# Kernel optimization log

Hardware: AMD Instinct MI355X
Metric: run time of the kernel (lower is better)

## Reference

```python
import jax, jax.numpy as jnp
import numpy as np

N_EMBD = 1024
HEAD_SIZE = 64


def setup_inputs() -> dict:
    key = jax.random.key(0)
    k1, k2, k3, k4 = jax.random.split(key, 4)
    x = jax.random.normal(k1, (8, 2048, N_EMBD), dtype=jnp.float32)
    # torch Linear(n_embd, head_size, bias=False): y = x @ W.T with W [out,in].
    # Store as [in, out] so y = x @ W. Scale init like torch default (~1/sqrt(in)).
    s = 1.0 / np.sqrt(N_EMBD)
    Wk = jax.random.uniform(k2, (N_EMBD, HEAD_SIZE), jnp.float32, -s, s)
    Wq = jax.random.uniform(k3, (N_EMBD, HEAD_SIZE), jnp.float32, -s, s)
    Wv = jax.random.uniform(k4, (N_EMBD, HEAD_SIZE), jnp.float32, -s, s)
    return {"x": x, "Wk": Wk, "Wq": Wq, "Wv": Wv}


def reference(x, Wk, Wq, Wv):
    # x: [B,T,C]
    B, T, C = x.shape
    k = x @ Wk  # [B,T,H]
    q = x @ Wq  # [B,T,H]
    v = x @ Wv  # [B,T,H]
    scale = HEAD_SIZE ** -0.5
    wei = jnp.einsum('bth,bsh->bts', q, k) * scale  # [B,T,T]
    causal = jnp.tril(jnp.ones((T, T), dtype=bool))  # [T,T]
    wei = jnp.where(causal[None, :, :], wei, -jnp.inf)
    wei = jax.nn.softmax(wei, axis=-1)
    # dropout(p=0.2) is identity in eval mode (deterministic baseline)
    out = jnp.einsum('bts,bsh->bth', wei, v)  # [B,T,H]
    return out
```

## Files before the change

kernel.cpp:

```cpp
#include <hip/hip_runtime.h>
#include <hip/hip_bf16.h>

#define B_DIM 8
#define T_DIM 2048
#define C_DIM 1024
#define H_DIM 64
#define BT (B_DIM * T_DIM)

typedef __attribute__((ext_vector_type(8))) short bf16x8;
typedef __attribute__((ext_vector_type(4))) float f32x4;

__device__ __forceinline__ ushort f2bf(float f) {
    __hip_bfloat16 h = __float2bfloat16(f);
    return *reinterpret_cast<ushort*>(&h);
}
__device__ __forceinline__ unsigned int packbf(float a, float b) {
    return (unsigned int)f2bf(a) | ((unsigned int)f2bf(b) << 16);
}

__global__ __launch_bounds__(256) void wt_convert_kernel(
    const float* __restrict__ Wk, const float* __restrict__ Wq,
    const float* __restrict__ Wv, ushort* __restrict__ wt)
{
    __shared__ float tile[64][65];
    const int mat = blockIdx.x >> 4;
    const int s   = blockIdx.x & 15;
    const int k0  = s << 6;
    const float* src = (mat == 0) ? Wk : (mat == 1) ? Wq : Wv;
    const float scale = (mat == 1) ? 0.125f * 1.4426950408889634f : 1.0f;
    #pragma unroll
    for (int i = 0; i < 16; ++i) {
        const int idx = i * 256 + threadIdx.x;
        const int r = idx >> 6, c = idx & 63;
        tile[r][c] = src[(size_t)(k0 + r) * H_DIM + c];
    }
    __syncthreads();
    const int ntl = threadIdx.x >> 6, lane = threadIdx.x & 63;
    const int col = lane & 15, quad = lane >> 4;
    const int nt = mat * 4 + ntl;
    const int w = nt / 3, j = nt % 3;
    #pragma unroll
    for (int ks = 0; ks < 2; ++ks) {
        unsigned int u[4];
        #pragma unroll
        for (int p = 0; p < 4; ++p)
            u[p] = packbf(tile[ks * 32 + quad * 8 + 2 * p][ntl * 16 + col] * scale,
                          tile[ks * 32 + quad * 8 + 2 * p + 1][ntl * 16 + col] * scale);
        ushort* dst = wt + (size_t)((((s * 4 + w) * 3 + j) * 2 + ks) * 512) + lane * 8;
        *(uint4*)dst = (uint4){u[0], u[1], u[2], u[3]};
    }
}

__global__ __launch_bounds__(256) void qkv_gemm_kernel(
    const float* __restrict__ x, const ushort* __restrict__ wt,
    ushort* __restrict__ kb, ushort* __restrict__ qb, ushort* __restrict__ vt)
{
    __shared__ ushort Xf[2][4 * 64 * 8];
    const int tid = threadIdx.x;
    const int wave = tid >> 6, lane = tid & 63;
    const int col = lane & 15, quad = lane >> 4;
    const int r0 = blockIdx.x * 32;

    f32x4 acc[2][3];
    #pragma unroll
    for (int m = 0; m < 2; ++m)
        #pragma unroll
        for (int i = 0; i < 3; ++i) acc[m][i] = (f32x4){0.f, 0.f, 0.f, 0.f};

    const int xrow = (wave >> 1) * 16 + col;
    const int xcc  = (wave & 1) * 4 + quad;
    const float* xsrc = x + (size_t)(r0 + xrow) * C_DIM + xcc * 8;

    const ushort* wsrc[3][2];
    #pragma unroll
    for (int j = 0; j < 3; ++j)
        #pragma unroll
        for (int ks = 0; ks < 2; ++ks)
            wsrc[j][ks] = wt + (size_t)(((wave * 3 + j) * 2 + ks) * 512) + lane * 8;

    {
        const float4 f0 = *(const float4*)(xsrc);
        const float4 f1 = *(const float4*)(xsrc + 4);
        uint4 u;
        u.x = packbf(f0.x, f0.y); u.y = packbf(f0.z, f0.w);
        u.z = packbf(f1.x, f1.y); u.w = packbf(f1.z, f1.w);
        *(uint4*)&Xf[0][(wave * 64 + lane) * 8] = u;
    }
    float4 xp[2][2];
    xp[0][0] = *(const float4*)(xsrc + 64);
    xp[0][1] = *(const float4*)(xsrc + 68);
    xp[1][0] = *(const float4*)(xsrc + 128);
    xp[1][1] = *(const float4*)(xsrc + 132);
    bf16x8 wcur[3][2];
    #pragma unroll
    for (int j = 0; j < 3; ++j)
        #pragma unroll
        for (int ks = 0; ks < 2; ++ks)
            wcur[j][ks] = *(const bf16x8*)(wsrc[j][ks]);
    __syncthreads();

    for (int i = 0; i < 16; ++i) {
        const int b = i & 1;
        const int sl = i & 1;
        if (i < 15) {
            uint4 u;
            u.x = packbf(xp[sl][0].x, xp[sl][0].y);
            u.y = packbf(xp[sl][0].z, xp[sl][0].w);
            u.z = packbf(xp[sl][1].x, xp[sl][1].y);
            u.w = packbf(xp[sl][1].z, xp[sl][1].w);
            *(uint4*)&Xf[b ^ 1][(wave * 64 + lane) * 8] = u;
        }
        bf16x8 wnxt[3][2];
        if (i < 15) {
            const size_t wo = (size_t)(i + 1) * 12288;
            #pragma unroll
            for (int j = 0; j < 3; ++j)
                #pragma unroll
                for (int ks = 0; ks < 2; ++ks)
                    wnxt[j][ks] = *(const bf16x8*)(wsrc[j][ks] + wo);
        }
        if (i + 3 < 16) {
            xp[sl][0] = *(const float4*)(xsrc + (i + 3) * 64);
            xp[sl][1] = *(const float4*)(xsrc + (i + 3) * 64 + 4);
        }
        #pragma unroll
        for (int ks = 0; ks < 2; ++ks) {
            const bf16x8 a0 = *(const bf16x8*)&Xf[b][((    ks) * 64 + lane) * 8];
            const bf16x8 a1 = *(const bf16x8*)&Xf[b][((2 + ks) * 64 + lane) * 8];
            #pragma unroll
            for (int j = 0; j < 3; ++j) {
                acc[0][j] = __builtin_amdgcn_mfma_f32_16x16x32_bf16(a0, wcur[j][ks], acc[0][j], 0, 0, 0);
                acc[1][j] = __builtin_amdgcn_mfma_f32_16x16x32_bf16(a1, wcur[j][ks], acc[1][j], 0, 0, 0);
            }
        }
        if (i < 15) {
            #pragma unroll
            for (int j = 0; j < 3; ++j)
                #pragma unroll
                for (int ks = 0; ks < 2; ++ks)
                    wcur[j][ks] = wnxt[j][ks];
        }
        asm volatile("s_waitcnt lgkmcnt(0)" ::: "memory");
        __builtin_amdgcn_sched_barrier(0);
        __builtin_amdgcn_s_barrier();
        __builtin_amdgcn_sched_barrier(0);
        asm volatile("" ::: "memory");
    }

    #pragma unroll
    for (int i = 0; i < 3; ++i) {
        const int nt = wave * 3 + i;
        #pragma unroll
        for (int mf = 0; mf < 2; ++mf) {
            const int rbase = r0 + mf * 16 + quad * 4;
            if (nt < 4) {
                const int n = nt * 16 + col;
                #pragma unroll
                for (int r = 0; r < 4; ++r)
                    kb[(size_t)(rbase + r) * H_DIM + n] = f2bf(acc[mf][i][r]);
            } else if (nt < 8) {
                const int n = nt * 16 + col - 64;
                #pragma unroll
                for (int r = 0; r < 4; ++r)
                    qb[(size_t)(rbase + r) * H_DIM + n] = f2bf(acc[mf][i][r]);
            } else {
                const int h = nt * 16 + col - 128;
                const int vbatch = rbase >> 11, vrow = rbase & (T_DIM - 1);
                ushort u4[4] = {f2bf(acc[mf][i][0]), f2bf(acc[mf][i][1]),
                                f2bf(acc[mf][i][2]), f2bf(acc[mf][i][3])};
                unsigned long long uu; __builtin_memcpy(&uu, u4, 8);
                *(unsigned long long*)(vt + ((size_t)vbatch * H_DIM + h) * T_DIM + vrow) = uu;
            }
        }
    }
}

__global__ __launch_bounds__(256) void attn_kernel(
    const ushort* __restrict__ kb, const ushort* __restrict__ qb,
    const ushort* __restrict__ vt, float* __restrict__ out)
{
    __shared__ ushort Kt[2][64][64];
    __shared__ ushort Vt[2][64][64];
    __shared__ unsigned int Ps[4][16 * 34];

    const int tid = threadIdx.x;
    const int wave = tid >> 6, lane = tid & 63;
    const int col = lane & 15, quad = lane >> 4;
    const int batch = blockIdx.x & 7;
    const int qt = 31 - (blockIdx.x >> 3);
    const int q0 = qt * 64;
    const int ntiles = qt + 1;
    const int qmy = q0 + wave * 16;

    const ushort* kbase = kb + (size_t)batch * T_DIM * H_DIM;
    const ushort* vbase = vt + (size_t)batch * H_DIM * T_DIM;

    const int srow0 = tid >> 3, srow1 = 32 + (tid >> 3);
    const int scb = tid & 7;
    const int sdst0 = (scb ^ (srow0 & 7)) * 8;
    const int sdst1 = (scb ^ (srow1 & 7)) * 8;

    const size_t qoff = (size_t)(batch * T_DIM + qmy + col) * H_DIM + quad * 8;
    const bf16x8 bq0 = *(const bf16x8*)(qb + qoff);
    const bf16x8 bq1 = *(const bf16x8*)(qb + qoff + 32);

    float l_ = 0.f;
    f32x4 o_[4];
    #pragma unroll
    for (int i = 0; i < 4; ++i) o_[i] = (f32x4){0.f, 0.f, 0.f, 0.f};

    unsigned int* psw = &Ps[wave][0];

    {
        const uint4 a0 = *(const uint4*)(kbase + (size_t)srow0 * H_DIM + scb * 8);
        const uint4 a1 = *(const uint4*)(kbase + (size_t)srow1 * H_DIM + scb * 8);
        const uint4 b0 = *(const uint4*)(vbase + (size_t)srow0 * T_DIM + scb * 8);
        const uint4 b1 = *(const uint4*)(vbase + (size_t)srow1 * T_DIM + scb * 8);
        *(uint4*)&Kt[0][srow0][sdst0] = a0;
        *(uint4*)&Kt[0][srow1][sdst1] = a1;
        *(uint4*)&Vt[0][srow0][sdst0] = b0;
        *(uint4*)&Vt[0][srow1][sdst1] = b1;
    }
    __syncthreads();

    for (int t = 0; t < ntiles; ++t) {
        const int b = t & 1;
        const int kb0 = t * 64;
        const bool pf = (t + 1 < ntiles);
        uint4 nk0, nk1, nv0, nv1;
        if (pf) {
            const int kb1 = kb0 + 64;
            nk0 = *(const uint4*)(kbase + (size_t)(kb1 + srow0) * H_DIM + scb * 8);
            nk1 = *(const uint4*)(kbase + (size_t)(kb1 + srow1) * H_DIM + scb * 8);
            nv0 = *(const uint4*)(vbase + (size_t)srow0 * T_DIM + kb1 + scb * 8);
            nv1 = *(const uint4*)(vbase + (size_t)srow1 * T_DIM + kb1 + scb * 8);
        }
        f32x4 s[4];
        #pragma unroll
        for (int mt = 0; mt < 4; ++mt) s[mt] = (f32x4){0.f, 0.f, 0.f, 0.f};
        __builtin_amdgcn_s_setprio(1);
        #pragma unroll
        for (int ks = 0; ks < 2; ++ks) {
            const bf16x8 bq = ks ? bq1 : bq0;
            #pragma unroll
            for (int mt = 0; mt < 4; ++mt) {
                const int row = mt * 16 + col;
                const bf16x8 ak = *(const bf16x8*)&Kt[b][row][((ks * 4 + quad) ^ (row & 7)) * 8];
                s[mt] = __builtin_amdgcn_mfma_f32_16x16x32_bf16(ak, bq, s[mt], 0, 0, 0);
            }
        }
        __builtin_amdgcn_s_setprio(0);
        if (kb0 + 63 > qmy) {
            const int kq = kb0 + quad * 4 - qmy - col;
            #pragma unroll
            for (int mt = 0; mt < 4; ++mt)
                #pragma unroll
                for (int reg = 0; reg < 4; ++reg)
                    if (kq + mt * 16 + reg > 0) s[mt][reg] = -INFINITY;
        }
        float psum[4];
        #pragma unroll
        for (int mt = 0; mt < 4; ++mt) {
            #pragma unroll
            for (int reg = 0; reg < 4; ++reg)
                s[mt][reg] = __builtin_amdgcn_exp2f(s[mt][reg]);
            psum[mt] = (s[mt][0] + s[mt][1]) + (s[mt][2] + s[mt][3]);
        }
        l_ += (psum[0] + psum[1]) + (psum[2] + psum[3]);
        #pragma unroll
        for (int mt = 0; mt < 4; ++mt) {
            uint2 w2;
            w2.x = packbf(s[mt][0], s[mt][1]);
            w2.y = packbf(s[mt][2], s[mt][3]);
            *(uint2*)&psw[col * 34 + mt * 8 + quad * 2] = w2;
        }
        __builtin_amdgcn_s_setprio(1);
        #pragma unroll
        for (int ks2 = 0; ks2 < 2; ++ks2) {
            const uint2 ra = *(const uint2*)&psw[col * 34 + ks2 * 16 + quad * 4];
            const uint2 rb = *(const uint2*)&psw[col * 34 + ks2 * 16 + quad * 4 + 2];
            unsigned int ub[4] = {ra.x, ra.y, rb.x, rb.y};
            bf16x8 bp; __builtin_memcpy(&bp, ub, 16);
            #pragma unroll
            for (int ht = 0; ht < 4; ++ht) {
                const int row = ht * 16 + col;
                const bf16x8 av = *(const bf16x8*)&Vt[b][row][((ks2 * 4 + quad) ^ (row & 7)) * 8];
                o_[ht] = __builtin_amdgcn_mfma_f32_16x16x32_bf16(av, bp, o_[ht], 0, 0, 0);
            }
        }
        __builtin_amdgcn_s_setprio(0);
        if (pf) {
            *(uint4*)&Kt[b ^ 1][srow0][sdst0] = nk0;
            *(uint4*)&Kt[b ^ 1][srow1][sdst1] = nk1;
            *(uint4*)&Vt[b ^ 1][srow0][sdst0] = nv0;
            *(uint4*)&Vt[b ^ 1][srow1][sdst1] = nv1;
        }
        __syncthreads();
    }

    float lt = l_;
    lt += __shfl_xor(lt, 16);
    lt += __shfl_xor(lt, 32);
    const float rL = 1.0f / lt;
    float* orow = out + (size_t)(batch * T_DIM + qmy + col) * H_DIM;
    #pragma unroll
    for (int ht = 0; ht < 4; ++ht)
        #pragma unroll
        for (int reg = 0; reg < 4; ++reg)
            orow[ht * 16 + quad * 4 + reg] = o_[ht][reg] * rL;
}

extern "C" void kernel_launch(void* const* d_in, const int* in_sizes, int n_in,
                              void* d_out, int out_size, void* d_ws, size_t ws_size,
                              hipStream_t stream)
{
    const float* x  = (const float*)d_in[0];
    const float* Wk = (const float*)d_in[1];
    const float* Wq = (const float*)d_in[2];
    const float* Wv = (const float*)d_in[3];

    ushort* kbuf = (ushort*)d_ws;
    ushort* qbuf = kbuf + (size_t)BT * H_DIM;
    ushort* vtb  = qbuf + (size_t)BT * H_DIM;
    ushort* wt   = vtb  + (size_t)BT * H_DIM;

    wt_convert_kernel<<<48, 256, 0, stream>>>(Wk, Wq, Wv, wt);
    qkv_gemm_kernel<<<BT / 32, 256, 0, stream>>>(x, wt, kbuf, qbuf, vtb);
    attn_kernel<<<B_DIM * 32, 256, 0, stream>>>(kbuf, qbuf, vtb, (float*)d_out);
}
```

Baseline: 150.1 us.

## Split KV tiles across waves with 16-row query blocks and LDS reduction

Each attention block now handles 16 query rows instead of 64, and its four waves take alternating 64-key tiles. Partial outputs and row sums are combined through shared memory at the end. K and V are loaded directly from global memory into registers, so the LDS double buffering and per-tile barriers go away. The grid grows fourfold to improve CU occupancy and causal load balance, at the cost of redundant K/V reads served from cache and no explicit prefetch.

```diff
diff --git a/kernel.cpp b/kernel.cpp
--- a/kernel.cpp
+++ b/kernel.cpp
@@ -175,32 +175,25 @@
     }
 }
 
-__global__ __launch_bounds__(256) void attn_kernel(
+__global__ __launch_bounds__(256, 4) void attn_kernel(
     const ushort* __restrict__ kb, const ushort* __restrict__ qb,
     const ushort* __restrict__ vt, float* __restrict__ out)
 {
-    __shared__ ushort Kt[2][64][64];
-    __shared__ ushort Vt[2][64][64];
     __shared__ unsigned int Ps[4][16 * 34];
+    __shared__ float Om[4][64][17];
+    __shared__ float Lm[4][16];
 
     const int tid = threadIdx.x;
     const int wave = tid >> 6, lane = tid & 63;
     const int col = lane & 15, quad = lane >> 4;
     const int batch = blockIdx.x & 7;
-    const int qt = 31 - (blockIdx.x >> 3);
-    const int q0 = qt * 64;
-    const int ntiles = qt + 1;
-    const int qmy = q0 + wave * 16;
+    const int qtile = 127 - (blockIdx.x >> 3);
+    const int q0 = qtile * 16;
 
     const ushort* kbase = kb + (size_t)batch * T_DIM * H_DIM;
     const ushort* vbase = vt + (size_t)batch * H_DIM * T_DIM;
 
-    const int srow0 = tid >> 3, srow1 = 32 + (tid >> 3);
-    const int scb = tid & 7;
-    const int sdst0 = (scb ^ (srow0 & 7)) * 8;
-    const int sdst1 = (scb ^ (srow1 & 7)) * 8;
-
-    const size_t qoff = (size_t)(batch * T_DIM + qmy + col) * H_DIM + quad * 8;
+    const size_t qoff = (size_t)(batch * T_DIM + q0 + col) * H_DIM + quad * 8;
     const bf16x8 bq0 = *(const bf16x8*)(qb + qoff);
     const bf16x8 bq1 = *(const bf16x8*)(qb + qoff + 32);
 
@@ -209,32 +202,25 @@
     #pragma unroll
     for (int i = 0; i < 4; ++i) o_[i] = (f32x4){0.f, 0.f, 0.f, 0.f};
 
+    const int ntiles = (q0 + 16 + 63) >> 6;
     unsigned int* psw = &Ps[wave][0];
 
-    {
-        const uint4 a0 = *(const uint4*)(kbase + (size_t)srow0 * H_DIM + scb * 8);
-        const uint4 a1 = *(const uint4*)(kbase + (size_t)srow1 * H_DIM + scb * 8);
-        const uint4 b0 = *(const uint4*)(vbase + (size_t)srow0 * T_DIM + scb * 8);
-        const uint4 b1 = *(const uint4*)(vbase + (size_t)srow1 * T_DIM + scb * 8);
-        *(uint4*)&Kt[0][srow0][sdst0] = a0;
-        *(uint4*)&Kt[0][srow1][sdst1] = a1;
-        *(uint4*)&Vt[0][srow0][sdst0] = b0;
-        *(uint4*)&Vt[0][srow1][sdst1] = b1;
-    }
-    __syncthreads();
-
-    for (int t = 0; t < ntiles; ++t) {
-        const int b = t & 1;
+    for (int t = wave; t < ntiles; t += 4) {
         const int kb0 = t * 64;
-        const bool pf = (t + 1 < ntiles);
-        uint4 nk0, nk1, nv0, nv1;
-        if (pf) {
-            const int kb1 = kb0 + 64;
-            nk0 = *(const uint4*)(kbase + (size_t)(kb1 + srow0) * H_DIM + scb * 8);
-            nk1 = *(const uint4*)(kbase + (size_t)(kb1 + srow1) * H_DIM + scb * 8);
-            nv0 = *(const uint4*)(vbase + (size_t)srow0 * T_DIM + kb1 + scb * 8);
-            nv1 = *(const uint4*)(vbase + (size_t)srow1 * T_DIM + kb1 + scb * 8);
-        }
+        bf16x8 ak[2][4];
+        #pragma unroll
+        for (int ks = 0; ks < 2; ++ks)
+            #pragma unroll
+            for (int mt = 0; mt < 4; ++mt)
+                ak[ks][mt] = *(const bf16x8*)
+                    (kbase + (size_t)(kb0 + mt * 16 + col) * H_DIM + ks * 32 + quad * 8);
+        bf16x8 av[2][4];
+        #pragma unroll
+        for (int ks2 = 0; ks2 < 2; ++ks2)
+            #pragma unroll
+            for (int ht = 0; ht < 4; ++ht)
+                av[ks2][ht] = *(const bf16x8*)
+                    (vbase + (size_t)(ht * 16 + col) * T_DIM + kb0 + ks2 * 32 + quad * 8);
         f32x4 s[4];
         #pragma unroll
         for (int mt = 0; mt < 4; ++mt) s[mt] = (f32x4){0.f, 0.f, 0.f, 0.f};
@@ -243,15 +229,12 @@
         for (int ks = 0; ks < 2; ++ks) {
             const bf16x8 bq = ks ? bq1 : bq0;
             #pragma unroll
-            for (int mt = 0; mt < 4; ++mt) {
-                const int row = mt * 16 + col;
-                const bf16x8 ak = *(const bf16x8*)&Kt[b][row][((ks * 4 + quad) ^ (row & 7)) * 8];
-                s[mt] = __builtin_amdgcn_mfma_f32_16x16x32_bf16(ak, bq, s[mt], 0, 0, 0);
-            }
+            for (int mt = 0; mt < 4; ++mt)
+                s[mt] = __builtin_amdgcn_mfma_f32_16x16x32_bf16(ak[ks][mt], bq, s[mt], 0, 0, 0);
         }
         __builtin_amdgcn_s_setprio(0);
-        if (kb0 + 63 > qmy) {
-            const int kq = kb0 + quad * 4 - qmy - col;
+        if (kb0 + 63 > q0) {
+            const int kq = kb0 + quad * 4 - q0 - col;
             #pragma unroll
             for (int mt = 0; mt < 4; ++mt)
                 #pragma unroll
@@ -282,32 +265,33 @@
             unsigned int ub[4] = {ra.x, ra.y, rb.x, rb.y};
             bf16x8 bp; __builtin_memcpy(&bp, ub, 16);
             #pragma unroll
-            for (int ht = 0; ht < 4; ++ht) {
-                const int row = ht * 16 + col;
-                const bf16x8 av = *(const bf16x8*)&Vt[b][row][((ks2 * 4 + quad) ^ (row & 7)) * 8];
-                o_[ht] = __builtin_amdgcn_mfma_f32_16x16x32_bf16(av, bp, o_[ht], 0, 0, 0);
-            }
+            for (int ht = 0; ht < 4; ++ht)
+                o_[ht] = __builtin_amdgcn_mfma_f32_16x16x32_bf16(av[ks2][ht], bp, o_[ht], 0, 0, 0);
         }
         __builtin_amdgcn_s_setprio(0);
-        if (pf) {
-            *(uint4*)&Kt[b ^ 1][srow0][sdst0] = nk0;
-            *(uint4*)&Kt[b ^ 1][srow1][sdst1] = nk1;
-            *(uint4*)&Vt[b ^ 1][srow0][sdst0] = nv0;
-            *(uint4*)&Vt[b ^ 1][srow1][sdst1] = nv1;
-        }
-        __syncthreads();
     }
 
     float lt = l_;
     lt += __shfl_xor(lt, 16);
     lt += __shfl_xor(lt, 32);
-    const float rL = 1.0f / lt;
-    float* orow = out + (size_t)(batch * T_DIM + qmy + col) * H_DIM;
     #pragma unroll
     for (int ht = 0; ht < 4; ++ht)
         #pragma unroll
         for (int reg = 0; reg < 4; ++reg)
-            orow[ht * 16 + quad * 4 + reg] = o_[ht][reg] * rL;
+            Om[wave][ht * 16 + quad * 4 + reg][col] = o_[ht][reg];
+    if (lane < 16) Lm[wave][lane] = lt;
+    __syncthreads();
+    {
+        const int q = tid >> 4, hb = tid & 15;
+        const float L = Lm[0][q] + Lm[1][q] + Lm[2][q] + Lm[3][q];
+        const float rL = 1.0f / L;
+        float* orow = out + (size_t)(batch * T_DIM + q0 + q) * H_DIM;
+        #pragma unroll
+        for (int i = 0; i < 4; ++i) {
+            const int h = hb + 16 * i;
+            orow[h] = (Om[0][h][q] + Om[1][h][q] + Om[2][h][q] + Om[3][h][q]) * rL;
+        }
+    }
 }
 
 extern "C" void kernel_launch(void* const* d_in, const int* in_sizes, int n_in,
@@ -326,5 +310,5 @@
 
     wt_convert_kernel<<<48, 256, 0, stream>>>(Wk, Wq, Wv, wt);
     qkv_gemm_kernel<<<BT / 32, 256, 0, stream>>>(x, wt, kbuf, qbuf, vtb);
-    attn_kernel<<<B_DIM * 32, 256, 0, stream>>>(kbuf, qbuf, vtb, (float*)d_out);
-}
+    attn_kernel<<<B_DIM * 128, 256, 0, stream>>>(kbuf, qbuf, vtb, (float*)d_out);
+}
```

After: 154.6 us. 3.0% more time.
